# Performance work log

Measured on AMD Instinct MI355X. Metric: run time of the kernel, lower is better.

The kernel has to match this reference:

```python
import jax, jax.numpy as jnp
import numpy as np

N, E, D, F, H = 20000, 600000, 128, 128, 4
C = 2 * D + F  # concat(source, sink, edge) feature dim


def _ln(x, g, b, eps=1e-5):
    mu = jnp.mean(x, -1, keepdims=True)
    v = jnp.mean((x - mu) ** 2, -1, keepdims=True)
    return (x - mu) / jnp.sqrt(v + eps) * g + b


def _gelu(x):
    return jax.nn.gelu(x, approximate=False)  # torch default exact GELU


def setup_inputs() -> dict:
    key = jax.random.key(0)
    ks = iter(jax.random.split(key, 40))

    def nrm(shape, s=0.05):
        return jax.random.normal(next(ks), shape, dtype=jnp.float32) * s

    inp = {}
    inp["bb_nodes"] = jax.random.normal(next(ks), (N, D), dtype=jnp.float32)
    inp["eattr"] = jax.random.normal(next(ks), (E, F), dtype=jnp.float32)
    inp["eidx"] = jax.random.randint(next(ks), (2, E), 0, N)
    inp["aW_w"] = nrm((H, D, C)); inp["aW_b"] = nrm((H, D))
    inp["aA_w"] = nrm((H, D));    inp["aA_b"] = nrm((H,))
    inp["nw1"] = nrm((D, C)); inp["nb1"] = nrm((D,))
    inp["nw2"] = nrm((D, D)); inp["nb2"] = nrm((D,))
    inp["nw3"] = nrm((D, D)); inp["nb3"] = nrm((D,))
    inp["dw1"] = nrm((4 * D, D)); inp["db1"] = nrm((4 * D,))
    inp["dw2"] = nrm((D, 4 * D)); inp["db2"] = nrm((D,))
    inp["ew1"] = nrm((F, C)); inp["eb1"] = nrm((F,))
    inp["ew2"] = nrm((F, F)); inp["eb2"] = nrm((F,))
    inp["ew3"] = nrm((F, F)); inp["eb3"] = nrm((F,))
    inp["aggr_w"] = nrm((D, H * D)); inp["aggr_b"] = nrm((D,))
    inp["ln1_g"] = jnp.ones((D,), jnp.float32); inp["ln1_b"] = jnp.zeros((D,), jnp.float32)
    inp["lne_g"] = jnp.ones((F,), jnp.float32); inp["lne_b"] = jnp.zeros((F,), jnp.float32)
    return inp


def reference(bb_nodes, eattr, eidx, aW_w, aW_b, aA_w, aA_b,
              nw1, nb1, nw2, nb2, nw3, nb3,
              dw1, db1, dw2, db2,
              ew1, eb1, ew2, eb2, ew3, eb3,
              aggr_w, aggr_b, ln1_g, ln1_b, lne_g, lne_b):
    n = bb_nodes.shape[0]
    src, snk = eidx[0], eidx[1]
    h = jnp.concatenate([bb_nodes[src], bb_nodes[snk], eattr], axis=1)  # [E, 2D+F]
    nheads = aW_w.shape[0]
    # per-head GAT-style logits; loop over small fixed head count to keep
    # peak memory at [E, D] per head rather than [H, E, D]
    logits = jnp.stack(
        [jax.nn.leaky_relu(h @ aW_w[k].T + aW_b[k], 0.2) @ aA_w[k] + aA_b[k]
         for k in range(nheads)], axis=1)                              # [E, H]
    msg = _gelu(h @ nw1.T + nb1)
    msg = _gelu(msg @ nw2.T + nb2)
    msg = msg @ nw3.T + nb3                                            # [E, D]
    # segment softmax over incoming edges of each sink node
    smax = jax.ops.segment_max(logits, snk, num_segments=n)            # [N, H]
    att = jnp.exp(logits - smax[snk])                                  # [E, H]
    norm = jax.ops.segment_sum(att + 1e-12, snk, num_segments=n)       # [N, H]
    att = att / norm[snk]
    # NOTE: faithful to the original's `atten[:, eidx[1]]` which re-gathers
    # the per-EDGE attention along the edge axis using NODE indices.
    att_g = att[snk]                                                   # [E, H]
    agg = jnp.stack(
        [jax.ops.segment_sum(att_g[:, k, None] * msg, snk, num_segments=n)
         for k in range(nheads)], axis=1)                              # [N, H, D]
    upd = agg.reshape(n, -1) @ aggr_w.T + aggr_b                       # [N, D]
    x = _ln(bb_nodes + upd, ln1_g, ln1_b)
    dense = _gelu(x @ dw1.T + db1) @ dw2.T + db2
    # original adds the attention update (not x) in the second residual,
    # and reuses node_norm1 both times (node_norm2 is dead code)
    x = _ln(dense + upd, ln1_g, ln1_b)
    eu = jnp.concatenate([x[src], x[snk], eattr], axis=1)              # [E, 2D+F]
    eu = _gelu(eu @ ew1.T + eb1)
    eu = _gelu(eu @ ew2.T + eb2)
    eu = eu @ ew3.T + eb3
    eout = _ln(eattr + eu, lne_g, lne_b)
    return x, eout
```

## Files before the change

### kernel.cpp

```cpp
#include <hip/hip_runtime.h>
#include <hip/hip_bf16.h>

#define N_NODES 20000
#define N_EDGES 600000
#define HEADS 4
#define MAXDEG 128

#define WOFF_AW   0
#define WOFF_NW1  196608
#define WOFF_NW2  245760
#define WOFF_NW3  262144
#define WOFF_EW1  278528
#define WOFF_EW2  327680
#define WOFF_EW3  344064
#define WOFF_AG   360448
#define WOFF_DW1  425984
#define WOFF_DW2  491520
#define WPACK_TOT 557056

typedef __attribute__((ext_vector_type(8))) short s16x8;
typedef __attribute__((ext_vector_type(4))) float f32x4;
typedef unsigned int u32;
typedef unsigned short u16;

__device__ __forceinline__ float bf2f(u16 h){ return __uint_as_float(((u32)h)<<16); }
__device__ __forceinline__ u16 f2bf(float f){
  u32 u = __float_as_uint(f) + 0x8000u;
  return (u16)(u>>16);
}
__device__ __forceinline__ float gelu_f(float x){
  float z2 = 1.5957691216057308f*(x + 0.044715f*x*x*x);
  float e = __expf(z2);
  float th = 1.f - 2.f/(e + 1.f);
  return 0.5f*x*(1.f + th);
}

__device__ __forceinline__ int swzf(int row){ return (row&15)<<4; }

__global__ __launch_bounds__(256) void k_pack(
    const float* __restrict__ aW, const float* __restrict__ nw1, const float* __restrict__ nw2,
    const float* __restrict__ nw3, const float* __restrict__ ew1, const float* __restrict__ ew2,
    const float* __restrict__ ew3, const float* __restrict__ aggr_w, const float* __restrict__ dw1,
    const float* __restrict__ dw2, const float* __restrict__ bb,
    u16* __restrict__ wpk, u16* __restrict__ bbp,
    float* __restrict__ norm, u32* __restrict__ cnt)
{
  int i = blockIdx.x*256 + threadIdx.x;
  if (i < WPACK_TOT){
    const float* src; int rel; int KROW;
    if      (i < WOFF_NW1){ src=aW;     rel=i;           KROW=384; }
    else if (i < WOFF_NW2){ src=nw1;    rel=i-WOFF_NW1;  KROW=384; }
    else if (i < WOFF_NW3){ src=nw2;    rel=i-WOFF_NW2;  KROW=128; }
    else if (i < WOFF_EW1){ src=nw3;    rel=i-WOFF_NW3;  KROW=128; }
    else if (i < WOFF_EW2){ src=ew1;    rel=i-WOFF_EW1;  KROW=384; }
    else if (i < WOFF_EW3){ src=ew2;    rel=i-WOFF_EW2;  KROW=128; }
    else if (i < WOFF_AG) { src=ew3;    rel=i-WOFF_EW3;  KROW=128; }
    else if (i < WOFF_DW1){ src=aggr_w; rel=i-WOFF_AG;   KROW=512; }
    else if (i < WOFF_DW2){ src=dw1;    rel=i-WOFF_DW1;  KROW=128; }
    else                  { src=dw2;    rel=i-WOFF_DW2;  KROW=512; }
    int e = rel&7, lane = (rel>>3)&63, frag = rel>>9;
    int ks, g;
    if      (KROW==384){ ks = frag % 12; g = frag / 12; }
    else if (KROW==128){ ks = frag & 3;  g = frag >> 2; }
    else               { ks = frag & 15; g = frag >> 4; }
    int row = g*16 + (lane&15);
    int k   = ks*32 + ((lane>>4)&3)*8 + e;
    wpk[i] = f2bf(src[(size_t)row*KROW + k]);
  }
  if (i < N_NODES*128) bbp[i] = f2bf(bb[i]);
  if (i < N_NODES*HEADS) norm[i] = 0.f;
  if (i < N_NODES) cnt[i] = 0u;
}

template<int NT, int KS, int RS>
__device__ __forceinline__ void gemmF(const char* ab, const u16* __restrict__ wfrag,
                                      int g0, int l, f32x4 (&acc)[4][NT])
{
  const int l15 = l&15, lg = l>>4;
  const int swz = l15<<4;
  const u16* wl = wfrag + l*8;
  #pragma unroll 4
  for (int ks=0; ks<KS; ++ks){
    s16x8 af[4];
    #pragma unroll
    for (int mt=0;mt<4;++mt)
      af[mt] = *(const s16x8*)(ab + (mt*16+l15)*RS + (((ks*4+lg)*16) ^ swz));
    #pragma unroll
    for (int nt=0;nt<NT;++nt){
      s16x8 bf = *(const s16x8*)(wl + (size_t)((g0+nt)*KS + ks)*512);
      #pragma unroll
      for (int mt=0;mt<4;++mt)
        acc[mt][nt] = __builtin_amdgcn_mfma_f32_16x16x32_bf16(af[mt], bf, acc[mt][nt], 0,0,0);
    }
  }
}

template<int KSI, int RS, int KSTOT>
__device__ __forceinline__ void gemmF2(const char* ab, const u16* __restrict__ wfrag,
                                       int g0, int ks0, int l, f32x4 (&acc)[4][1])
{
  const int l15 = l&15, lg = l>>4;
  const int swz = l15<<4;
  const u16* wl = wfrag + l*8;
  #pragma unroll 4
  for (int ks=0; ks<KSI; ++ks){
    s16x8 af[4];
    #pragma unroll
    for (int mt=0;mt<4;++mt)
      af[mt] = *(const s16x8*)(ab + (mt*16+l15)*RS + (((ks*4+lg)*16) ^ swz));
    s16x8 bf = *(const s16x8*)(wl + (size_t)(g0*KSTOT + ks0 + ks)*512);
    #pragma unroll
    for (int mt=0;mt<4;++mt)
      acc[mt][0] = __builtin_amdgcn_mfma_f32_16x16x32_bf16(af[mt], bf, acc[mt][0], 0,0,0);
  }
}

template<int RS>
__device__ __forceinline__ void writeReg(char* hsb, int regionByte, int col, int lg,
                                         const float (&v)[4][4])
{
  #pragma unroll
  for (int mt=0;mt<4;++mt){
    #pragma unroll
    for (int r=0;r<4;++r){
      int row = mt*16 + lg*4 + r;
      *(u16*)(hsb + row*RS + regionByte + ((col*2) ^ swzf(row))) = f2bf(v[mt][r]);
    }
  }
}

__device__ __forceinline__ void stage512(char* hsb, const u16* __restrict__ ntab,
                                         const float* __restrict__ eattr, const int* __restrict__ eidx,
                                         int e0, int t)
{
  const int row = t>>3, p = t&7, ge = e0+row;
  const int swz = swzf(row);
  char* rp = hsb + row*768;
  if (p < 4){
    int nid = eidx[(p<2 ? 0 : N_EDGES) + ge];
    const int4* srow = (const int4*)(ntab + (size_t)nid*128);
    const int base = (p<2) ? 0 : 16;
    #pragma unroll
    for (int s=0;s<8;++s){
      int ci = (2*s + p) & 15;
      int4 v = srow[ci];
      *(int4*)(rp + (((base+ci)*16) ^ swz)) = v;
    }
  } else {
    int q = p-4;
    const float* er = eattr + (size_t)ge*128 + q*32;
    #pragma unroll
    for (int c=0;c<4;++c){
      float4 x0 = ((const float4*)er)[c*2];
      float4 x1 = ((const float4*)er)[c*2+1];
      int4 v;
      v.x = (int)((u32)f2bf(x0.x) | ((u32)f2bf(x0.y)<<16));
      v.y = (int)((u32)f2bf(x0.z) | ((u32)f2bf(x0.w)<<16));
      v.z = (int)((u32)f2bf(x1.x) | ((u32)f2bf(x1.y)<<16));
      v.w = (int)((u32)f2bf(x1.z) | ((u32)f2bf(x1.w)<<16));
      *(int4*)(rp + (((32 + q*4 + c)*16) ^ swz)) = v;
    }
  }
}

__global__ __launch_bounds__(512,4) void k_edgeA(
  const u16* __restrict__ bbp, const float* __restrict__ eattr, const int* __restrict__ eidx,
  const u16* __restrict__ wpk,
  const float* __restrict__ aW_b, const float* __restrict__ aA_w, const float* __restrict__ aA_b,
  const float* __restrict__ nb1, const float* __restrict__ nb2, const float* __restrict__ nb3,
  float* __restrict__ logits, float* __restrict__ norm, u32* __restrict__ cnt,
  int* __restrict__ eids2, u16* __restrict__ msg)
{
  __shared__ u16 hs[64*384];
  __shared__ float lpart[8*64];
  __shared__ int snkid[64];
  char* hsb = (char*)hs;
  const int t = threadIdx.x;
  const int e0 = blockIdx.x*64;
  const int w = t>>6, l = t&63, l15 = l&15, lg = l>>4;
  const int col = w*16 + l15;

  stage512(hsb, bbp, eattr, eidx, e0, t);
  lpart[w*64 + l] = 0.f;
  if (t < 64){
    int k = eidx[N_EDGES + e0 + t];
    snkid[t] = k;
    u32 pos = atomicAdd(&cnt[k], 1u);
    if (pos < MAXDEG) eids2[k*MAXDEG + pos] = e0 + t;
  }
  __syncthreads();

  {
    #pragma unroll
    for (int ch=0; ch<2; ++ch){
      f32x4 acc[4][2];
      #pragma unroll
      for (int mt=0;mt<4;++mt){
        #pragma unroll
        for (int nt=0;nt<2;++nt){ f32x4 z={0.f,0.f,0.f,0.f}; acc[mt][nt]=z; }
      }
      int g0 = (w>>1)*8 + (w&1)*4 + ch*2;
      gemmF<2,12,768>(hsb, wpk+WOFF_AW, g0, l, acc);
      float lp[4][4];
      #pragma unroll
      for (int a=0;a<4;++a){
        #pragma unroll
        for (int b=0;b<4;++b) lp[a][b]=0.f;
      }
      #pragma unroll
      for (int nt=0;nt<2;++nt){
        int gcol = (w>>1)*128 + (w&1)*64 + ch*32 + nt*16 + l15;
        float bia = aW_b[gcol];
        float avw = aA_w[gcol];
        #pragma unroll
        for (int mt=0;mt<4;++mt){
          #pragma unroll
          for (int r=0;r<4;++r){
            float T = acc[mt][nt][r] + bia;
            T = fmaxf(T, 0.2f*T);
            lp[mt][r] += T*avw;
          }
        }
      }
      #pragma unroll
      for (int mt=0;mt<4;++mt){
        #pragma unroll
        for (int r=0;r<4;++r){
          float v = lp[mt][r];
          v += __shfl_xor(v,1);
          v += __shfl_xor(v,2);
          v += __shfl_xor(v,4);
          v += __shfl_xor(v,8);
          if (l15==0) lpart[w*64 + mt*16 + lg*4 + r] += v;
        }
      }
    }
  }
  float m1v[4][4];
  {
    f32x4 acc[4][1];
    #pragma unroll
    for (int mt=0;mt<4;++mt){ f32x4 z={0.f,0.f,0.f,0.f}; acc[mt][0]=z; }
    gemmF<1,12,768>(hsb, wpk+WOFF_NW1, w, l, acc);
    float b = nb1[col];
    #pragma unroll
    for (int mt=0;mt<4;++mt){
      #pragma unroll
      for (int r=0;r<4;++r) m1v[mt][r] = gelu_f(acc[mt][0][r] + b);
    }
  }
  __syncthreads();

  if (t < 256){
    int row = t>>2, h = t&3;
    float s = lpart[(2*h)*64 + row] + lpart[(2*h+1)*64 + row] + aA_b[h];
    int e = e0 + row;
    if (e0 < N_NODES) logits[e*HEADS + h] = s;
    atomicAdd(&norm[snkid[row]*HEADS + h], expf(s));
  }
  writeReg<768>(hsb, 0, col, lg, m1v);
  __syncthreads();

  {
    f32x4 acc[4][1];
    #pragma unroll
    for (int mt=0;mt<4;++mt){ f32x4 z={0.f,0.f,0.f,0.f}; acc[mt][0]=z; }
    gemmF<1,4,768>(hsb, wpk+WOFF_NW2, w, l, acc);
    float b = nb2[col];
    float v[4][4];
    #pragma unroll
    for (int mt=0;mt<4;++mt){
      #pragma unroll
      for (int r=0;r<4;++r) v[mt][r] = gelu_f(acc[mt][0][r] + b);
    }
    writeReg<768>(hsb, 256, col, lg, v);
  }
  __syncthreads();

  {
    f32x4 acc[4][1];
    #pragma unroll
    for (int mt=0;mt<4;++mt){ f32x4 z={0.f,0.f,0.f,0.f}; acc[mt][0]=z; }
    gemmF<1,4,768>(hsb+256, wpk+WOFF_NW3, w, l, acc);
    float b = nb3[col];
    float v[4][4];
    #pragma unroll
    for (int mt=0;mt<4;++mt){
      #pragma unroll
      for (int r=0;r<4;++r) v[mt][r] = acc[mt][0][r] + b;
    }
    writeReg<768>(hsb, 512, col, lg, v);
  }
  __syncthreads();

  {
    int row = t>>3, p = t&7;
    const int swz = swzf(row);
    #pragma unroll
    for (int c=0;c<2;++c){
      int j = c*8 + p;
      int4 v = *(const int4*)(hsb + row*768 + 512 + ((j*16) ^ swz));
      *(int4*)((char*)msg + (size_t)(e0+row)*256 + j*16) = v;
    }
  }
}

__global__ __launch_bounds__(256) void k_msgsumZ(
  const u16* __restrict__ msg, const int* __restrict__ eids2, const u32* __restrict__ cnt,
  const int* __restrict__ eidx, const float* __restrict__ logits,
  const float* __restrict__ norm,
  u16* __restrict__ z)
{
  __shared__ float red[4][128];
  __shared__ float av[4];
  const int n = blockIdx.x, t = threadIdx.x;
  u32* zrow = (u32*)z + (size_t)n*256;
  if (n >= N_NODES){
    zrow[t] = 0u;
    return;
  }
  const int w = t>>6, l = t&63;
  int ecnt = (int)cnt[n]; if (ecnt > MAXDEG) ecnt = MAXDEG;
  float a0=0.f, a1=0.f;
  for (int i=w; i<ecnt; i+=4){
    int e = eids2[n*MAXDEG + i];
    u32 v = *(const u32*)(msg + (size_t)e*128 + l*2);
    a0 += __uint_as_float(v<<16);
    a1 += __uint_as_float(v & 0xFFFF0000u);
  }
  red[w][l*2] = a0; red[w][l*2+1] = a1;
  if (t < 4){
    int sn = eidx[N_EDGES + n];
    float c = 1e-12f * (float)cnt[sn];
    av[t] = expf(logits[n*HEADS+t]) / (norm[sn*HEADS+t] + c);
  }
  __syncthreads();
  int h = t>>6, dp = (t&63)*2;
  float s0 = red[0][dp]+red[1][dp]+red[2][dp]+red[3][dp];
  float s1 = red[0][dp+1]+red[1][dp+1]+red[2][dp+1]+red[3][dp+1];
  float a = av[h];
  zrow[h*64 + (t&63)] = (u32)f2bf(a*s0) | ((u32)f2bf(a*s1)<<16);
}

__global__ __launch_bounds__(512,2) void k_node(
  const u16* __restrict__ z, const float* __restrict__ bb,
  const u16* __restrict__ wpk, const float* __restrict__ aggr_b,
  const float* __restrict__ db1, const float* __restrict__ db2,
  const float* __restrict__ lng, const float* __restrict__ lnb,
  float* __restrict__ xout, u16* __restrict__ xbp)
{
  __shared__ u16 hs[64*512];
  __shared__ float lps[8*64];
  __shared__ float lpss[8*64];
  __shared__ float mrs[2*64];
  char* hsb = (char*)hs;
  const int t = threadIdx.x;
  const int nbase = blockIdx.x*64;
  const int w = t>>6, l = t&63, l15 = l&15, lg = l>>4;
  const int col = w*16 + l15;

  {
    const int row = t>>3, p = t&7;
    const int swz = swzf(row);
    char* rp = hsb + row*1024;
    const int4* zr = (const int4*)((const char*)z + (size_t)(nbase+row)*1024);
    #pragma unroll
    for (int c=0;c<8;++c){
      int ci = c*8 + p;
      int4 v = zr[ci];
      *(int4*)(rp + ((ci*16) ^ swz)) = v;
    }
  }
  __syncthreads();

  float v[4][4];
  {
    f32x4 acc[4][1];
    #pragma unroll
    for (int mt=0;mt<4;++mt){ f32x4 z_={0.f,0.f,0.f,0.f}; acc[mt][0]=z_; }
    gemmF<1,16,1024>(hsb, wpk+WOFF_AG, w, l, acc);
    float ab = aggr_b[col];
    #pragma unroll
    for (int mt=0;mt<4;++mt){
      #pragma unroll
      for (int r=0;r<4;++r) v[mt][r] = acc[mt][0][r] + ab;
    }
  }
  __syncthreads();

  {
    float xv[4][4];
    #pragma unroll
    for (int mt=0;mt<4;++mt){
      #pragma unroll
      for (int r=0;r<4;++r){
        int row = mt*16 + lg*4 + r;
        int ge = nbase + row; if (ge >= N_NODES) ge = N_NODES-1;
        xv[mt][r] = bb[(size_t)ge*128 + col] + v[mt][r];
      }
    }
    #pragma unroll
    for (int mt=0;mt<4;++mt){
      #pragma unroll
      for (int r=0;r<4;++r){
        float a = xv[mt][r], b = xv[mt][r]*xv[mt][r];
        a += __shfl_xor(a,1); b += __shfl_xor(b,1);
        a += __shfl_xor(a,2); b += __shfl_xor(b,2);
        a += __shfl_xor(a,4); b += __shfl_xor(b,4);
        a += __shfl_xor(a,8); b += __shfl_xor(b,8);
        if (l15==0){
          int row = mt*16 + lg*4 + r;
          lps[w*64 + row] = a;
          lpss[w*64 + row] = b;
        }
      }
    }
    __syncthreads();
    if (t < 64){
      float a=0.f, b=0.f;
      #pragma unroll
      for (int j=0;j<8;++j){ a += lps[j*64+t]; b += lpss[j*64+t]; }
      float mu = a*(1.f/128.f);
      float var = b*(1.f/128.f) - mu*mu;
      mrs[t] = mu;
      mrs[64+t] = rsqrtf(var + 1e-5f);
    }
    __syncthreads();
    float g = lng[col], bt = lnb[col];
    float xb[4][4];
    #pragma unroll
    for (int mt=0;mt<4;++mt){
      #pragma unroll
      for (int r=0;r<4;++r){
        int row = mt*16 + lg*4 + r;
        xb[mt][r] = (xv[mt][r] - mrs[row])*mrs[64+row]*g + bt;
      }
    }
    writeReg<1024>(hsb, 0, col, lg, xb);
  }
  __syncthreads();

  f32x4 acc3[4][1];
  #pragma unroll
  for (int mt=0;mt<4;++mt){ f32x4 z_={0.f,0.f,0.f,0.f}; acc3[mt][0]=z_; }
  #pragma unroll
  for (int c=0;c<4;++c){
    {
      f32x4 acc[4][1];
      #pragma unroll
      for (int mt=0;mt<4;++mt){ f32x4 z_={0.f,0.f,0.f,0.f}; acc[mt][0]=z_; }
      gemmF<1,4,1024>(hsb, wpk+WOFF_DW1, c*8 + w, l, acc);
      float b1 = db1[c*128 + col];
      float dh[4][4];
      #pragma unroll
      for (int mt=0;mt<4;++mt){
        #pragma unroll
        for (int r=0;r<4;++r) dh[mt][r] = gelu_f(acc[mt][0][r] + b1);
      }
      writeReg<1024>(hsb, 256 + (c&1)*256, col, lg, dh);
    }
    __syncthreads();
    gemmF2<4,1024,16>(hsb + 256 + (c&1)*256, wpk+WOFF_DW2, w, c*4, l, acc3);
  }

  {
    float ov[4][4];
    float b2 = db2[col];
    #pragma unroll
    for (int mt=0;mt<4;++mt){
      #pragma unroll
      for (int r=0;r<4;++r) ov[mt][r] = acc3[mt][0][r] + b2 + v[mt][r];
    }
    #pragma unroll
    for (int mt=0;mt<4;++mt){
      #pragma unroll
      for (int r=0;r<4;++r){
        float a = ov[mt][r], b = ov[mt][r]*ov[mt][r];
        a += __shfl_xor(a,1); b += __shfl_xor(b,1);
        a += __shfl_xor(a,2); b += __shfl_xor(b,2);
        a += __shfl_xor(a,4); b += __shfl_xor(b,4);
        a += __shfl_xor(a,8); b += __shfl_xor(b,8);
        if (l15==0){
          int row = mt*16 + lg*4 + r;
          lps[w*64 + row] = a;
          lpss[w*64 + row] = b;
        }
      }
    }
    __syncthreads();
    if (t < 64){
      float a=0.f, b=0.f;
      #pragma unroll
      for (int j=0;j<8;++j){ a += lps[j*64+t]; b += lpss[j*64+t]; }
      float mu = a*(1.f/128.f);
      float var = b*(1.f/128.f) - mu*mu;
      mrs[t] = mu;
      mrs[64+t] = rsqrtf(var + 1e-5f);
    }
    __syncthreads();
    float g = lng[col], bt = lnb[col];
    #pragma unroll
    for (int mt=0;mt<4;++mt){
      #pragma unroll
      for (int r=0;r<4;++r){
        int row = mt*16 + lg*4 + r;
        int ge = nbase + row;
        if (ge < N_NODES){
          float o = (ov[mt][r] - mrs[row])*mrs[64+row]*g + bt;
          xout[(size_t)ge*128 + col] = o;
          xbp[(size_t)ge*128 + col] = f2bf(o);
        }
      }
    }
  }
}

__global__ __launch_bounds__(512,4) void k_edgeC(
  const u16* __restrict__ xbp, const float* __restrict__ eattr, const int* __restrict__ eidx,
  const u16* __restrict__ wpk,
  const float* __restrict__ eb1, const float* __restrict__ eb2, const float* __restrict__ eb3,
  const float* __restrict__ lng, const float* __restrict__ lnb,
  float* __restrict__ eout)
{
  __shared__ u16 hs[64*384];
  __shared__ float wps[8*64];
  __shared__ float wpss[8*64];
  __shared__ float mrs[2*64];
  char* hsb=(char*)hs;
  const int t = threadIdx.x;
  const int e0 = blockIdx.x*64;
  const int w = t>>6, l = t&63, l15 = l&15, lg = l>>4;
  const int col = w*16 + l15;

  stage512(hsb, xbp, eattr, eidx, e0, t);
  __syncthreads();

  float e1v[4][4];
  {
    f32x4 acc[4][1];
    #pragma unroll
    for (int mt=0;mt<4;++mt){ f32x4 z={0.f,0.f,0.f,0.f}; acc[mt][0]=z; }
    gemmF<1,12,768>(hsb, wpk+WOFF_EW1, w, l, acc);
    float b = eb1[col];
    #pragma unroll
    for (int mt=0;mt<4;++mt){
      #pragma unroll
      for (int r=0;r<4;++r) e1v[mt][r] = gelu_f(acc[mt][0][r] + b);
    }
  }
  __syncthreads();
  writeReg<768>(hsb, 0, col, lg, e1v);
  __syncthreads();

  {
    f32x4 acc[4][1];
    #pragma unroll
    for (int mt=0;mt<4;++mt){ f32x4 z={0.f,0.f,0.f,0.f}; acc[mt][0]=z; }
    gemmF<1,4,768>(hsb, wpk+WOFF_EW2, w, l, acc);
    float b = eb2[col];
    float v[4][4];
    #pragma unroll
    for (int mt=0;mt<4;++mt){
      #pragma unroll
      for (int r=0;r<4;++r) v[mt][r] = gelu_f(acc[mt][0][r] + b);
    }
    writeReg<768>(hsb, 256, col, lg, v);
  }
  __syncthreads();

  {
    f32x4 acc[4][1];
    #pragma unroll
    for (int mt=0;mt<4;++mt){ f32x4 z={0.f,0.f,0.f,0.f}; acc[mt][0]=z; }
    gemmF<1,4,768>(hsb+256, wpk+WOFF_EW3, w, l, acc);
    float b3 = eb3[col];
    float v[4][4];
    #pragma unroll
    for (int mt=0;mt<4;++mt){
      #pragma unroll
      for (int r=0;r<4;++r){
        int row = mt*16 + lg*4 + r;
        float ea = bf2f(*(const u16*)(hsb + row*768 + 512 + ((col*2) ^ swzf(row))));
        v[mt][r] = acc[mt][0][r] + b3 + ea;
      }
    }
    #pragma unroll
    for (int mt=0;mt<4;++mt){
      #pragma unroll
      for (int r=0;r<4;++r){
        float a = v[mt][r], b = v[mt][r]*v[mt][r];
        a += __shfl_xor(a,1); b += __shfl_xor(b,1);
        a += __shfl_xor(a,2); b += __shfl_xor(b,2);
        a += __shfl_xor(a,4); b += __shfl_xor(b,4);
        a += __shfl_xor(a,8); b += __shfl_xor(b,8);
        if (l15==0){
          int row = mt*16 + lg*4 + r;
          wps[w*64 + row] = a;
          wpss[w*64 + row] = b;
        }
      }
    }
    __syncthreads();
    if (t < 64){
      float a=0.f, b=0.f;
      #pragma unroll
      for (int j=0;j<8;++j){ a += wps[j*64+t]; b += wpss[j*64+t]; }
      float mu = a*(1.f/128.f);
      float var = b*(1.f/128.f) - mu*mu;
      mrs[t] = mu;
      mrs[64+t] = rsqrtf(var + 1e-5f);
    }
    __syncthreads();
    float g = lng[col], bb_ = lnb[col];
    #pragma unroll
    for (int mt=0;mt<4;++mt){
      #pragma unroll
      for (int r=0;r<4;++r){
        int row = mt*16 + lg*4 + r;
        float o = (v[mt][r] - mrs[row])*mrs[64+row]*g + bb_;
        eout[(size_t)(e0+row)*128 + col] = o;
      }
    }
  }
}

static inline size_t alup(size_t x){ return (x + 255) & ~(size_t)255; }

extern "C" void kernel_launch(void* const* d_in, const int* in_sizes, int n_in,
                              void* d_out, int out_size, void* d_ws, size_t ws_size,
                              hipStream_t stream)
{
  (void)in_sizes; (void)n_in; (void)out_size; (void)ws_size;
  const float* bb    = (const float*)d_in[0];
  const float* eattr = (const float*)d_in[1];
  const int*   eidx  = (const int*)d_in[2];
  const float* aW_w  = (const float*)d_in[3];
  const float* aW_b  = (const float*)d_in[4];
  const float* aA_w  = (const float*)d_in[5];
  const float* aA_b  = (const float*)d_in[6];
  const float* nw1   = (const float*)d_in[7];
  const float* nb1   = (const float*)d_in[8];
  const float* nw2   = (const float*)d_in[9];
  const float* nb2   = (const float*)d_in[10];
  const float* nw3   = (const float*)d_in[11];
  const float* nb3   = (const float*)d_in[12];
  const float* dw1   = (const float*)d_in[13];
  const float* db1   = (const float*)d_in[14];
  const float* dw2   = (const float*)d_in[15];
  const float* db2   = (const float*)d_in[16];
  const float* ew1   = (const float*)d_in[17];
  const float* eb1   = (const float*)d_in[18];
  const float* ew2   = (const float*)d_in[19];
  const float* eb2   = (const float*)d_in[20];
  const float* ew3   = (const float*)d_in[21];
  const float* eb3   = (const float*)d_in[22];
  const float* aggr_w= (const float*)d_in[23];
  const float* aggr_b= (const float*)d_in[24];
  const float* ln1g  = (const float*)d_in[25];
  const float* ln1b  = (const float*)d_in[26];
  const float* lneg  = (const float*)d_in[27];
  const float* lneb  = (const float*)d_in[28];

  char* p = (char*)d_ws;
  auto take = [&](size_t bytes)->char*{ char* r = p; p += alup(bytes); return r; };
  u16*   wpk    = (u16*)  take((size_t)WPACK_TOT*2);
  u16*   bbp    = (u16*)  take((size_t)N_NODES*128*2);
  u16*   xbp    = (u16*)  take((size_t)N_NODES*128*2);
  float* logits = (float*)take((size_t)N_EDGES*HEADS*4);
  float* norm   = (float*)take((size_t)N_NODES*HEADS*4);
  u32*   cnt    = (u32*)  take((size_t)N_NODES*4);
  int*   eids2  = (int*)  take((size_t)N_NODES*MAXDEG*4);
  u16*   z      = (u16*)  take((size_t)20032*512*2);

  float* xout = (float*)d_out;
  float* eout = xout + (size_t)N_NODES*128;
  u16*   msg  = (u16*)eout;

  k_pack    <<<dim3(10000), dim3(256), 0, stream>>>(aW_w,nw1,nw2,nw3,ew1,ew2,ew3,aggr_w,dw1,dw2,bb,wpk,bbp,norm,cnt);
  k_edgeA   <<<dim3(9375),  dim3(512), 0, stream>>>(bbp,eattr,eidx,wpk,aW_b,aA_w,aA_b,nb1,nb2,nb3,logits,norm,cnt,eids2,msg);
  k_msgsumZ <<<dim3(20032), dim3(256), 0, stream>>>(msg,eids2,cnt,eidx,logits,norm,z);
  k_node    <<<dim3(313),   dim3(512), 0, stream>>>(z,bb,wpk,aggr_b,db1,db2,ln1g,ln1b,xout,xbp);
  k_edgeC   <<<dim3(9375),  dim3(512), 0, stream>>>(xbp,eattr,eidx,wpk,eb1,eb2,eb3,lneg,lneb,eout);
}
```

Before: 1.056 ms.

## Retile edge attention/message kernel to 32-edge blocks with 2x2 wave tiles

Halves the k_edgeA block to 32 edges and 256 threads and launches twice as many blocks. Each wave now computes a 2x2 MFMA tile, and for the attention GEMM each wave owns one full head. That removes the cross-wave summation of partial logits and the read-modify-write on lpart. The aim is more resident blocks and a smaller shared-memory footprint per block, at the cost of less reuse of each weight fragment (two MFMAs per B load instead of four) and more total weight traffic.

```diff
diff --git a/kernel.cpp b/kernel.cpp
--- a/kernel.cpp
+++ b/kernel.cpp
@@ -95,6 +95,29 @@
   }
 }
 
+template<int MT, int NT, int KS, int RS>
+__device__ __forceinline__ void gemmFM(const char* ab, const u16* __restrict__ wfrag,
+                                       int g0, int l, f32x4 (&acc)[MT][NT])
+{
+  const int l15 = l&15, lg = l>>4;
+  const int swz = l15<<4;
+  const u16* wl = wfrag + l*8;
+  #pragma unroll 4
+  for (int ks=0; ks<KS; ++ks){
+    s16x8 af[MT];
+    #pragma unroll
+    for (int mt=0;mt<MT;++mt)
+      af[mt] = *(const s16x8*)(ab + (mt*16+l15)*RS + (((ks*4+lg)*16) ^ swz));
+    #pragma unroll
+    for (int nt=0;nt<NT;++nt){
+      s16x8 bf = *(const s16x8*)(wl + (size_t)((g0+nt)*KS + ks)*512);
+      #pragma unroll
+      for (int mt=0;mt<MT;++mt)
+        acc[mt][nt] = __builtin_amdgcn_mfma_f32_16x16x32_bf16(af[mt], bf, acc[mt][nt], 0,0,0);
+    }
+  }
+}
+
 template<int KSI, int RS, int KSTOT>
 __device__ __forceinline__ void gemmF2(const char* ab, const u16* __restrict__ wfrag,
                                        int g0, int ks0, int l, f32x4 (&acc)[4][1])
@@ -125,6 +148,23 @@
     for (int r=0;r<4;++r){
       int row = mt*16 + lg*4 + r;
       *(u16*)(hsb + row*RS + regionByte + ((col*2) ^ swzf(row))) = f2bf(v[mt][r]);
+    }
+  }
+}
+
+__device__ __forceinline__ void writeReg22(char* hsb, int regionByte, int colbase,
+                                           int l15, int lg, const float (&v)[2][2][4])
+{
+  #pragma unroll
+  for (int mt=0;mt<2;++mt){
+    #pragma unroll
+    for (int nt=0;nt<2;++nt){
+      int col = colbase + nt*16 + l15;
+      #pragma unroll
+      for (int r=0;r<4;++r){
+        int row = mt*16 + lg*4 + r;
+        *(u16*)(hsb + row*768 + regionByte + ((col*2) ^ swzf(row))) = f2bf(v[mt][nt][r]);
+      }
     }
   }
 }
@@ -163,7 +203,7 @@
   }
 }
 
-__global__ __launch_bounds__(512,4) void k_edgeA(
+__global__ __launch_bounds__(256,4) void k_edgeA(
   const u16* __restrict__ bbp, const float* __restrict__ eattr, const int* __restrict__ eidx,
   const u16* __restrict__ wpk,
   const float* __restrict__ aW_b, const float* __restrict__ aA_w, const float* __restrict__ aA_b,
@@ -171,18 +211,17 @@
   float* __restrict__ logits, float* __restrict__ norm, u32* __restrict__ cnt,
   int* __restrict__ eids2, u16* __restrict__ msg)
 {
-  __shared__ u16 hs[64*384];
-  __shared__ float lpart[8*64];
-  __shared__ int snkid[64];
+  __shared__ u16 hs[32*384];
+  __shared__ float lpart[4*32];
+  __shared__ int snkid[32];
   char* hsb = (char*)hs;
   const int t = threadIdx.x;
-  const int e0 = blockIdx.x*64;
+  const int e0 = blockIdx.x*32;
   const int w = t>>6, l = t&63, l15 = l&15, lg = l>>4;
-  const int col = w*16 + l15;
+  const int colb = w*32;
 
   stage512(hsb, bbp, eattr, eidx, e0, t);
-  lpart[w*64 + l] = 0.f;
-  if (t < 64){
+  if (t < 32){
     int k = eidx[N_EDGES + e0 + t];
     snkid[t] = k;
     u32 pos = atomicAdd(&cnt[k], 1u);
@@ -191,29 +230,27 @@
   __syncthreads();
 
   {
-    #pragma unroll
-    for (int ch=0; ch<2; ++ch){
-      f32x4 acc[4][2];
-      #pragma unroll
-      for (int mt=0;mt<4;++mt){
+    float lp[2][4];
+    #pragma unroll
+    for (int a=0;a<2;++a){
+      #pragma unroll
+      for (int b=0;b<4;++b) lp[a][b]=0.f;
+    }
+    for (int ch=0; ch<4; ++ch){
+      f32x4 acc[2][2];
+      #pragma unroll
+      for (int mt=0;mt<2;++mt){
         #pragma unroll
         for (int nt=0;nt<2;++nt){ f32x4 z={0.f,0.f,0.f,0.f}; acc[mt][nt]=z; }
       }
-      int g0 = (w>>1)*8 + (w&1)*4 + ch*2;
-      gemmF<2,12,768>(hsb, wpk+WOFF_AW, g0, l, acc);
-      float lp[4][4];
-      #pragma unroll
-      for (int a=0;a<4;++a){
-        #pragma unroll
-        for (int b=0;b<4;++b) lp[a][b]=0.f;
-      }
+      gemmFM<2,2,12,768>(hsb, wpk+WOFF_AW, w*8 + ch*2, l, acc);
       #pragma unroll
       for (int nt=0;nt<2;++nt){
-        int gcol = (w>>1)*128 + (w&1)*64 + ch*32 + nt*16 + l15;
+        int gcol = w*128 + ch*32 + nt*16 + l15;
         float bia = aW_b[gcol];
         float avw = aA_w[gcol];
         #pragma unroll
-        for (int mt=0;mt<4;++mt){
+        for (int mt=0;mt<2;++mt){
           #pragma unroll
           for (int r=0;r<4;++r){
             float T = acc[mt][nt][r] + bia;
@@ -222,74 +259,92 @@
           }
         }
       }
-      #pragma unroll
-      for (int mt=0;mt<4;++mt){
+    }
+    #pragma unroll
+    for (int mt=0;mt<2;++mt){
+      #pragma unroll
+      for (int r=0;r<4;++r){
+        float v = lp[mt][r];
+        v += __shfl_xor(v,1);
+        v += __shfl_xor(v,2);
+        v += __shfl_xor(v,4);
+        v += __shfl_xor(v,8);
+        if (l15==0) lpart[w*32 + mt*16 + lg*4 + r] = v;
+      }
+    }
+  }
+  float m1v[2][2][4];
+  {
+    f32x4 acc[2][2];
+    #pragma unroll
+    for (int mt=0;mt<2;++mt){
+      #pragma unroll
+      for (int nt=0;nt<2;++nt){ f32x4 z={0.f,0.f,0.f,0.f}; acc[mt][nt]=z; }
+    }
+    gemmFM<2,2,12,768>(hsb, wpk+WOFF_NW1, w*2, l, acc);
+    #pragma unroll
+    for (int nt=0;nt<2;++nt){
+      float b = nb1[colb + nt*16 + l15];
+      #pragma unroll
+      for (int mt=0;mt<2;++mt){
         #pragma unroll
-        for (int r=0;r<4;++r){
-          float v = lp[mt][r];
-          v += __shfl_xor(v,1);
-          v += __shfl_xor(v,2);
-          v += __shfl_xor(v,4);
-          v += __shfl_xor(v,8);
-          if (l15==0) lpart[w*64 + mt*16 + lg*4 + r] += v;
-        }
-      }
-    }
-  }
-  float m1v[4][4];
-  {
-    f32x4 acc[4][1];
-    #pragma unroll
-    for (int mt=0;mt<4;++mt){ f32x4 z={0.f,0.f,0.f,0.f}; acc[mt][0]=z; }
-    gemmF<1,12,768>(hsb, wpk+WOFF_NW1, w, l, acc);
-    float b = nb1[col];
-    #pragma unroll
-    for (int mt=0;mt<4;++mt){
-      #pragma unroll
-      for (int r=0;r<4;++r) m1v[mt][r] = gelu_f(acc[mt][0][r] + b);
-    }
-  }
-  __syncthreads();
-
-  if (t < 256){
+        for (int r=0;r<4;++r) m1v[mt][nt][r] = gelu_f(acc[mt][nt][r] + b);
+      }
+    }
+  }
+  __syncthreads();
+
+  if (t < 128){
     int row = t>>2, h = t&3;
-    float s = lpart[(2*h)*64 + row] + lpart[(2*h+1)*64 + row] + aA_b[h];
+    float s = lpart[h*32 + row] + aA_b[h];
     int e = e0 + row;
     if (e0 < N_NODES) logits[e*HEADS + h] = s;
     atomicAdd(&norm[snkid[row]*HEADS + h], expf(s));
   }
-  writeReg<768>(hsb, 0, col, lg, m1v);
-  __syncthreads();
-
-  {
-    f32x4 acc[4][1];
-    #pragma unroll
-    for (int mt=0;mt<4;++mt){ f32x4 z={0.f,0.f,0.f,0.f}; acc[mt][0]=z; }
-    gemmF<1,4,768>(hsb, wpk+WOFF_NW2, w, l, acc);
-    float b = nb2[col];
-    float v[4][4];
-    #pragma unroll
-    for (int mt=0;mt<4;++mt){
-      #pragma unroll
-      for (int r=0;r<4;++r) v[mt][r] = gelu_f(acc[mt][0][r] + b);
-    }
-    writeReg<768>(hsb, 256, col, lg, v);
-  }
-  __syncthreads();
-
-  {
-    f32x4 acc[4][1];
-    #pragma unroll
-    for (int mt=0;mt<4;++mt){ f32x4 z={0.f,0.f,0.f,0.f}; acc[mt][0]=z; }
-    gemmF<1,4,768>(hsb+256, wpk+WOFF_NW3, w, l, acc);
-    float b = nb3[col];
-    float v[4][4];
-    #pragma unroll
-    for (int mt=0;mt<4;++mt){
-      #pragma unroll
-      for (int r=0;r<4;++r) v[mt][r] = acc[mt][0][r] + b;
-    }
-    writeReg<768>(hsb, 512, col, lg, v);
+  writeReg22(hsb, 0, colb, l15, lg, m1v);
+  __syncthreads();
+
+  {
+    f32x4 acc[2][2];
+    #pragma unroll
+    for (int mt=0;mt<2;++mt){
+      #pragma unroll
+      for (int nt=0;nt<2;++nt){ f32x4 z={0.f,0.f,0.f,0.f}; acc[mt][nt]=z; }
+    }
+    gemmFM<2,2,4,768>(hsb, wpk+WOFF_NW2, w*2, l, acc);
+    float v2[2][2][4];
+    #pragma unroll
+    for (int nt=0;nt<2;++nt){
+      float b = nb2[colb + nt*16 + l15];
+      #pragma unroll
+      for (int mt=0;mt<2;++mt){
+        #pragma unroll
+        for (int r=0;r<4;++r) v2[mt][nt][r] = gelu_f(acc[mt][nt][r] + b);
+      }
+    }
+    writeReg22(hsb, 256, colb, l15, lg, v2);
+  }
+  __syncthreads();
+
+  {
+    f32x4 acc[2][2];
+    #pragma unroll
+    for (int mt=0;mt<2;++mt){
+      #pragma unroll
+      for (int nt=0;nt<2;++nt){ f32x4 z={0.f,0.f,0.f,0.f}; acc[mt][nt]=z; }
+    }
+    gemmFM<2,2,4,768>(hsb+256, wpk+WOFF_NW3, w*2, l, acc);
+    float v3[2][2][4];
+    #pragma unroll
+    for (int nt=0;nt<2;++nt){
+      float b = nb3[colb + nt*16 + l15];
+      #pragma unroll
+      for (int mt=0;mt<2;++mt){
+        #pragma unroll
+        for (int r=0;r<4;++r) v3[mt][nt][r] = acc[mt][nt][r] + b;
+      }
+    }
+    writeReg22(hsb, 512, colb, l15, lg, v3);
   }
   __syncthreads();
 
@@ -677,7 +732,7 @@
   u16*   msg  = (u16*)eout;
 
   k_pack    <<<dim3(10000), dim3(256), 0, stream>>>(aW_w,nw1,nw2,nw3,ew1,ew2,ew3,aggr_w,dw1,dw2,bb,wpk,bbp,norm,cnt);
-  k_edgeA   <<<dim3(9375),  dim3(512), 0, stream>>>(bbp,eattr,eidx,wpk,aW_b,aA_w,aA_b,nb1,nb2,nb3,logits,norm,cnt,eids2,msg);
+  k_edgeA   <<<dim3(18750), dim3(256), 0, stream>>>(bbp,eattr,eidx,wpk,aW_b,aA_w,aA_b,nb1,nb2,nb3,logits,norm,cnt,eids2,msg);
   k_msgsumZ <<<dim3(20032), dim3(256), 0, stream>>>(msg,eids2,cnt,eidx,logits,norm,z);
   k_node    <<<dim3(313),   dim3(512), 0, stream>>>(z,bb,wpk,aggr_b,db1,db2,ln1g,ln1b,xout,xbp);
   k_edgeC   <<<dim3(9375),  dim3(512), 0, stream>>>(xbp,eattr,eidx,wpk,eb1,eb2,eb3,lneg,lneb,eout);
```

Result: slower. 1.144 ms (+8.4%).
